# Performance work log

Hardware: AMD Instinct MI355X
Metric: run time of the kernel (lower is better)

Reference implementation:

```python
import jax, jax.numpy as jnp
import numpy as np

VIEW_R = 32
SCALING = 16.0 / 8.0  # lora_alpha / r


def setup_inputs() -> dict:
    key = jax.random.key(0)
    ks = jax.random.split(key, 12)
    bs, S, d, r = 64, 256, 768, 8
    n = d // VIEW_R  # 24
    return {
        "x": jax.random.normal(ks[0], (bs, S, d), jnp.float32),
        "user_h": jax.random.normal(ks[1], (bs, d), jnp.float32),
        "item_h": jax.random.normal(ks[2], (bs, d), jnp.float32),
        "W": jax.random.normal(ks[3], (d, d), jnp.float32) * 0.02,   # base weight (out,in)
        "b": jax.random.normal(ks[4], (d,), jnp.float32) * 0.02,
        "A": jax.random.normal(ks[5], (r, d), jnp.float32) * 0.02,   # lora_A
        "B": jax.random.normal(ks[6], (d, r), jnp.float32) * 0.02,   # lora_B (zeros at init; randomized to exercise math)
        "Wu": jax.random.normal(ks[7], (d, d), jnp.float32) * 0.02,  # lora_U weight (out,in)
        "VU": jax.random.normal(ks[8], (n, VIEW_R), jnp.float32) * 0.02,
        "Wi": jax.random.normal(ks[9], (d, d), jnp.float32) * 0.02,  # lora_I weight
        "VI": jax.random.normal(ks[10], (n, VIEW_R), jnp.float32) * 0.02,
    }


def _kron_branch(x, h, Wlin, V):
    # original: weight[b, q*n_in + n, l*32 + m] = (h @ Wlin.T)[b, q, l] * V[n, m]
    #           result[b,s,:] = x[b,s,:] @ weight[b]
    # factorized form (same math, no (bs, d, d) intermediate):
    bs, S, d = x.shape
    n, m = V.shape
    q = VIEW_R
    l = d // VIEW_R
    wq = (h @ Wlin.T).reshape(bs, q, l)          # (b, q, l)
    x4 = x.reshape(bs, S, q, n)                  # d split as (q, n)
    t = jnp.einsum("bsqn,nm->bsqm", x4, V)
    out = jnp.einsum("bsqm,bql->bslm", t, wq)    # out index = l*32 + m
    return out.reshape(bs, S, d)


def reference(x, user_h, item_h, W, b, A, B, Wu, VU, Wi, VI):
    # F.linear + LoRA
    out = jnp.einsum("bsd,od->bso", x, W) + b
    out = out + jnp.einsum("bsd,rd,or->bso", x, A, B) * SCALING
    # user Kronecker low-rank per-sample weight branch
    out = out + _kron_branch(x, user_h, Wu, VU)
    # item branch
    out = out + _kron_branch(x, item_h, Wi, VI)
    return out
```

## Files before the change

### kernel.cpp

```cpp
#include <hip/hip_runtime.h>
#include <hip/hip_bf16.h>

typedef __bf16 bf16x8 __attribute__((ext_vector_type(8)));
typedef float f32x4 __attribute__((ext_vector_type(4)));
typedef unsigned short u16x8 __attribute__((ext_vector_type(8)));

__device__ __forceinline__ unsigned short f2bf(float f) {
    unsigned int u = __builtin_bit_cast(unsigned int, f);
    unsigned int r = (u + 0x7FFFu + ((u >> 16) & 1u)) >> 16;
    return (unsigned short)r;
}

__device__ __forceinline__ void load_lds_16(const void* g, void* lds) {
    __builtin_amdgcn_global_load_lds(
        (const __attribute__((address_space(1))) unsigned int*)g,
        (__attribute__((address_space(3))) unsigned int*)lds, 16, 0, 0);
}

__global__ void prep_kernel(const float* __restrict__ x, unsigned short* __restrict__ xb,
                            const float* __restrict__ W, const float* __restrict__ A,
                            const float* __restrict__ B, unsigned short* __restrict__ weffB,
                            const float* __restrict__ uh, const float* __restrict__ ih,
                            const float* __restrict__ Wu, const float* __restrict__ Wi,
                            float* __restrict__ wqu, float* __restrict__ wqi) {
    int bx = blockIdx.x;
    int t = threadIdx.x;
    if (bx < 6144) {
        int i = bx * 256 + t;
        const float4* xp = (const float4*)x;
        float4 a = xp[i * 2];
        float4 c = xp[i * 2 + 1];
        u16x8 r;
        r[0] = f2bf(a.x); r[1] = f2bf(a.y); r[2] = f2bf(a.z); r[3] = f2bf(a.w);
        r[4] = f2bf(c.x); r[5] = f2bf(c.y); r[6] = f2bf(c.z); r[7] = f2bf(c.w);
        *(u16x8*)(xb + (size_t)i * 8) = r;
    } else if (bx < 8448) {
        int idx = bx - 6144;
        int o = idx / 3;
        int k = (idx % 3) * 256 + t;
        float acc = W[o * 768 + k];
#pragma unroll
        for (int r = 0; r < 8; ++r) acc += 2.0f * B[o * 8 + r] * A[r * 768 + k];
        weffB[o * 768 + k] = f2bf(acc);
    } else {
        int b2 = bx - 8448;
        int og = b2 % 192;
        int rest = b2 / 192;
        int b = rest & 63;
        int br = rest >> 6;
        int wave = t >> 6, lane = t & 63;
        int o = og * 4 + wave;
        const float* h = (br ? ih : uh) + b * 768;
        const float* Wrow = (br ? Wi : Wu) + (size_t)o * 768;
        const float4* hp = (const float4*)(h + lane * 12);
        const float4* wp = (const float4*)(Wrow + lane * 12);
        float s = 0.0f;
#pragma unroll
        for (int j = 0; j < 3; ++j) {
            float4 hv = hp[j], wv = wp[j];
            s += hv.x * wv.x + hv.y * wv.y + hv.z * wv.z + hv.w * wv.w;
        }
#pragma unroll
        for (int off = 32; off; off >>= 1) s += __shfl_down(s, off);
        if (lane == 0) (br ? wqi : wqu)[b * 768 + o] = s;
    }
}

__global__ __launch_bounds__(256, 2) void gemm_fused_kernel(
    const unsigned short* __restrict__ Xb, const unsigned short* __restrict__ WeffB,
    const float* __restrict__ VU, const float* __restrict__ VI,
    const float* __restrict__ wqu, const float* __restrict__ wqi,
    const float* __restrict__ bias, float* __restrict__ out) {
    __shared__ __align__(16) unsigned short As[128 * 64];
    __shared__ __align__(16) unsigned short Bs[128 * 64];
    __shared__ __align__(16) unsigned short Ks[128 * 64];
    __shared__ __align__(16) float vui[32 * 26 * 2];
    __shared__ float wqs[4 * 32 * 2];
    __shared__ float bias_s[128];
    const int tid = threadIdx.x;
    const int wave = tid >> 6, lane = tid & 63;
    const int id = blockIdx.x;
    const int nt = id >> 7, rem = id & 127, b = rem >> 1, mt = rem & 1;
    const int s0 = mt * 128, n0 = nt * 128;

    for (int i = tid; i < 768; i += 256) {
        int n = i >> 5, m = i & 31;
        vui[(m * 26 + n) * 2] = VU[i];
        vui[(m * 26 + n) * 2 + 1] = VI[i];
    }
    if (tid < 128) {
        int q = tid >> 2, lr = tid & 3;
        int l = nt * 4 + lr;
        wqs[(lr * 32 + q) * 2] = wqu[b * 768 + q * 24 + l];
        wqs[(lr * 32 + q) * 2 + 1] = wqi[b * 768 + q * 24 + l];
        bias_s[tid] = bias[n0 + tid];
    }
    __syncthreads();

    const unsigned short* Abase = Xb + (size_t)(b * 256 + s0) * 768;
    const unsigned short* Bbase = WeffB + (size_t)n0 * 768;
    const int wm = wave & 1, wn = wave >> 1;
    const int lrow = lane >> 3, lcp = lane & 7;

    f32x4 acc[4][4] = {};

    for (int kk = 0; kk < 768; kk += 64) {
#pragma unroll
        for (int u = 0; u < 4; ++u) {
            int tA = wave * 4 + u;
            int r = tA * 8 + lrow;
            int c = lcp ^ (r & 7);
            load_lds_16(Abase + (size_t)r * 768 + kk + c * 8, (void*)(As + tA * 512));
            load_lds_16(Bbase + (size_t)r * 768 + kk + c * 8, (void*)(Bs + tA * 512));
            int kb = kk + c * 8;
            int q = (kb * 2731) >> 16;
            int n0c = kb - q * 24;
            int m = r & 31, lr = r >> 5;
            const float* vp = &vui[(m * 26 + n0c) * 2];
            float wu = wqs[(lr * 32 + q) * 2];
            float wi = wqs[(lr * 32 + q) * 2 + 1];
            u16x8 kv;
#pragma unroll
            for (int j = 0; j < 8; ++j)
                kv[j] = f2bf(vp[j * 2] * wu + vp[j * 2 + 1] * wi);
            *(u16x8*)(Ks + r * 64 + lcp * 8) = kv;
        }
        __syncthreads();
#pragma unroll
        for (int h = 0; h < 2; ++h) {
            const int cb = h * 4 + (lane >> 4);
            const int rl = lane & 15;
            bf16x8 af[4], bw[4], bk[4];
#pragma unroll
            for (int i = 0; i < 4; ++i) {
                int r = wm * 64 + i * 16 + rl;
                int c = cb ^ (r & 7);
                af[i] = *(const bf16x8*)(As + r * 64 + c * 8);
            }
#pragma unroll
            for (int j = 0; j < 4; ++j) {
                int r = wn * 64 + j * 16 + rl;
                int c = cb ^ (r & 7);
                bw[j] = *(const bf16x8*)(Bs + r * 64 + c * 8);
                bk[j] = *(const bf16x8*)(Ks + r * 64 + c * 8);
            }
#pragma unroll
            for (int i = 0; i < 4; ++i)
#pragma unroll
                for (int j = 0; j < 4; ++j) {
                    acc[i][j] = __builtin_amdgcn_mfma_f32_16x16x32_bf16(af[i], bw[j], acc[i][j], 0, 0, 0);
                    acc[i][j] = __builtin_amdgcn_mfma_f32_16x16x32_bf16(af[i], bk[j], acc[i][j], 0, 0, 0);
                }
        }
        __syncthreads();
    }

    const int cl = lane & 15, rq = lane >> 4;
#pragma unroll
    for (int j = 0; j < 4; ++j) {
        int nn = wn * 64 + j * 16 + cl;
        float bv = bias_s[nn];
#pragma unroll
        for (int i = 0; i < 4; ++i) {
            int mrow = s0 + wm * 64 + i * 16 + rq * 4;
            float* op = out + (size_t)(b * 256 + mrow) * 768 + n0 + nn;
#pragma unroll
            for (int g = 0; g < 4; ++g) op[(size_t)g * 768] = acc[i][j][g] + bv;
        }
    }
}

__global__ void weff_kernel(const float* __restrict__ W, const float* __restrict__ A,
                            const float* __restrict__ B, float* __restrict__ Weff) {
    int o = blockIdx.x / 3;
    int k = (blockIdx.x % 3) * 256 + threadIdx.x;
    float acc = W[o * 768 + k];
#pragma unroll
    for (int r = 0; r < 8; ++r) acc += 2.0f * B[o * 8 + r] * A[r * 768 + k];
    Weff[o * 768 + k] = acc;
}

__global__ void wq2_kernel(const float* __restrict__ uh, const float* __restrict__ ih,
                           const float* __restrict__ Wu, const float* __restrict__ Wi,
                           float* __restrict__ wqu, float* __restrict__ wqi) {
    int bx = blockIdx.x;
    int og = bx % 192;
    int rest = bx / 192;
    int b = rest & 63;
    int br = rest >> 6;
    int wave = threadIdx.x >> 6, lane = threadIdx.x & 63;
    int o = og * 4 + wave;
    const float* h = (br ? ih : uh) + b * 768;
    const float* Wrow = (br ? Wi : Wu) + (size_t)o * 768;
    const float4* hp = (const float4*)(h + lane * 12);
    const float4* wp = (const float4*)(Wrow + lane * 12);
    float s = 0.0f;
#pragma unroll
    for (int j = 0; j < 3; ++j) {
        float4 hv = hp[j], wv = wp[j];
        s += hv.x * wv.x + hv.y * wv.y + hv.z * wv.z + hv.w * wv.w;
    }
#pragma unroll
    for (int off = 32; off; off >>= 1) s += __shfl_down(s, off);
    if (lane == 0) (br ? wqi : wqu)[b * 768 + o] = s;
}

__global__ void naive_kernel(const float* __restrict__ x, const float* __restrict__ Weff,
                             const float* __restrict__ wqu, const float* __restrict__ wqi,
                             const float* __restrict__ VU, const float* __restrict__ VI,
                             const float* __restrict__ bias, float* __restrict__ out) {
    int bs_ = blockIdx.x / 3;
    int chunk = blockIdx.x % 3;
    int b = bs_ >> 8;
    __shared__ float xs[768];
    for (int i = threadIdx.x; i < 768; i += 256) xs[i] = x[(size_t)bs_ * 768 + i];
    __syncthreads();
    int o = chunk * 256 + threadIdx.x;
    int m = o & 31, l = o >> 5;
    float acc = bias[o];
    for (int q = 0; q < 32; ++q) {
        float wu = wqu[b * 768 + q * 24 + l];
        float wi = wqi[b * 768 + q * 24 + l];
#pragma unroll
        for (int n = 0; n < 24; ++n) {
            int k = q * 24 + n;
            float w = Weff[o * 768 + k] + VU[n * 32 + m] * wu + VI[n * 32 + m] * wi;
            acc += xs[k] * w;
        }
    }
    out[(size_t)bs_ * 768 + o] = acc;
}

extern "C" void kernel_launch(void* const* d_in, const int* in_sizes, int n_in,
                              void* d_out, int out_size, void* d_ws, size_t ws_size,
                              hipStream_t stream) {
    const float* x  = (const float*)d_in[0];
    const float* uh = (const float*)d_in[1];
    const float* ih = (const float*)d_in[2];
    const float* W  = (const float*)d_in[3];
    const float* bv = (const float*)d_in[4];
    const float* A  = (const float*)d_in[5];
    const float* B  = (const float*)d_in[6];
    const float* Wu = (const float*)d_in[7];
    const float* VU = (const float*)d_in[8];
    const float* Wi = (const float*)d_in[9];
    const float* VI = (const float*)d_in[10];
    float* out = (float*)d_out;

    const size_t off_xb   = 0;
    const size_t off_weff = 25165824;
    const size_t off_wqu  = off_weff + 1179648;
    const size_t off_wqi  = off_wqu + 196608;
    const size_t need     = off_wqi + 196608;

    char* ws = (char*)d_ws;
    if (ws_size >= need) {
        unsigned short* xb    = (unsigned short*)(ws + off_xb);
        unsigned short* weffB = (unsigned short*)(ws + off_weff);
        float* wqu = (float*)(ws + off_wqu);
        float* wqi = (float*)(ws + off_wqi);
        prep_kernel<<<33024, 256, 0, stream>>>(x, xb, W, A, B, weffB, uh, ih, Wu, Wi, wqu, wqi);
        gemm_fused_kernel<<<768, 256, 0, stream>>>(xb, weffB, VU, VI, wqu, wqi, bv, out);
    } else {
        float* weff = (float*)ws;
        float* wqu  = weff + 589824;
        float* wqi  = wqu + 49152;
        weff_kernel<<<2304, 256, 0, stream>>>(W, A, B, weff);
        wq2_kernel<<<24576, 256, 0, stream>>>(uh, ih, Wu, Wi, wqu, wqi);
        naive_kernel<<<49152, 256, 0, stream>>>(x, weff, wqu, wqi, VU, VI, bv, out);
    }
}
```

Baseline: 183.6 us.

## Pack V tables as bf16 pairs and share Kron-weight tile construction across rows

The VU/VI tables are stored in LDS as packed bf16 pairs, and the per-block wq values are reorganised so each thread builds four Kron-weight rows (one per l) from the same V slice. This cuts repeated LDS reads and conversions in the K-tile build inside the main loop. Rounding to bf16 is replaced by truncation, and launch bounds are raised to three blocks per SM, which lowers the register budget. V is now quantised to bf16 before the multiply, which slightly changes numerics.

```diff
diff --git a/kernel.cpp b/kernel.cpp
--- a/kernel.cpp
+++ b/kernel.cpp
@@ -66,7 +66,7 @@
     }
 }
 
-__global__ __launch_bounds__(256, 2) void gemm_fused_kernel(
+__global__ __launch_bounds__(256, 3) void gemm_fused_kernel(
     const unsigned short* __restrict__ Xb, const unsigned short* __restrict__ WeffB,
     const float* __restrict__ VU, const float* __restrict__ VI,
     const float* __restrict__ wqu, const float* __restrict__ wqi,
@@ -74,8 +74,8 @@
     __shared__ __align__(16) unsigned short As[128 * 64];
     __shared__ __align__(16) unsigned short Bs[128 * 64];
     __shared__ __align__(16) unsigned short Ks[128 * 64];
-    __shared__ __align__(16) float vui[32 * 26 * 2];
-    __shared__ float wqs[4 * 32 * 2];
+    __shared__ __align__(16) unsigned int vui[32 * 26];
+    __shared__ __align__(16) float wqs[32 * 8];
     __shared__ float bias_s[128];
     const int tid = threadIdx.x;
     const int wave = tid >> 6, lane = tid & 63;
@@ -85,22 +85,22 @@
 
     for (int i = tid; i < 768; i += 256) {
         int n = i >> 5, m = i & 31;
-        vui[(m * 26 + n) * 2] = VU[i];
-        vui[(m * 26 + n) * 2 + 1] = VI[i];
-    }
-    if (tid < 128) {
-        int q = tid >> 2, lr = tid & 3;
-        int l = nt * 4 + lr;
-        wqs[(lr * 32 + q) * 2] = wqu[b * 768 + q * 24 + l];
-        wqs[(lr * 32 + q) * 2 + 1] = wqi[b * 768 + q * 24 + l];
-        bias_s[tid] = bias[n0 + tid];
-    }
+        vui[m * 26 + n] = ((unsigned int)f2bf(VU[i]) << 16) | (unsigned int)f2bf(VI[i]);
+    }
+    {
+        int q = tid >> 3, lr = (tid >> 1) & 3, br = tid & 1;
+        const float* wq = br ? wqi : wqu;
+        wqs[tid] = wq[b * 768 + q * 24 + nt * 4 + lr];
+    }
+    if (tid < 128) bias_s[tid] = bias[n0 + tid];
     __syncthreads();
 
     const unsigned short* Abase = Xb + (size_t)(b * 256 + s0) * 768;
     const unsigned short* Bbase = WeffB + (size_t)n0 * 768;
     const int wm = wave & 1, wn = wave >> 1;
     const int lrow = lane >> 3, lcp = lane & 7;
+    const int mp = tid & 31, cp = tid >> 5;
+    const int psl = cp ^ (mp & 7);
 
     f32x4 acc[4][4] = {};
 
@@ -112,18 +112,35 @@
             int c = lcp ^ (r & 7);
             load_lds_16(Abase + (size_t)r * 768 + kk + c * 8, (void*)(As + tA * 512));
             load_lds_16(Bbase + (size_t)r * 768 + kk + c * 8, (void*)(Bs + tA * 512));
-            int kb = kk + c * 8;
+        }
+        {
+            int kb = kk + cp * 8;
             int q = (kb * 2731) >> 16;
             int n0c = kb - q * 24;
-            int m = r & 31, lr = r >> 5;
-            const float* vp = &vui[(m * 26 + n0c) * 2];
-            float wu = wqs[(lr * 32 + q) * 2];
-            float wi = wqs[(lr * 32 + q) * 2 + 1];
-            u16x8 kv;
-#pragma unroll
-            for (int j = 0; j < 8; ++j)
-                kv[j] = f2bf(vp[j * 2] * wu + vp[j * 2 + 1] * wi);
-            *(u16x8*)(Ks + r * 64 + lcp * 8) = kv;
+            const unsigned int* vp = &vui[mp * 26 + n0c];
+            uint2 pv01 = *(const uint2*)(vp);
+            uint2 pv23 = *(const uint2*)(vp + 2);
+            uint2 pv45 = *(const uint2*)(vp + 4);
+            uint2 pv67 = *(const uint2*)(vp + 6);
+            unsigned int pv[8] = {pv01.x, pv01.y, pv23.x, pv23.y, pv45.x, pv45.y, pv67.x, pv67.y};
+            float fu[8], fi[8];
+#pragma unroll
+            for (int j = 0; j < 8; ++j) {
+                fu[j] = __builtin_bit_cast(float, pv[j] & 0xFFFF0000u);
+                fi[j] = __builtin_bit_cast(float, pv[j] << 16);
+            }
+            const float2* wp = (const float2*)&wqs[q * 8];
+#pragma unroll
+            for (int lr = 0; lr < 4; ++lr) {
+                float2 w = wp[lr];
+                u16x8 kv;
+#pragma unroll
+                for (int j = 0; j < 8; ++j) {
+                    float v = fu[j] * w.x + fi[j] * w.y;
+                    kv[j] = (unsigned short)(__builtin_bit_cast(unsigned int, v) >> 16);
+                }
+                *(u16x8*)(Ks + (lr * 32 + mp) * 64 + psl * 8) = kv;
+            }
         }
         __syncthreads();
 #pragma unroll
```

Result: faster. 177.1 us (-3.5%).
